# Kernel optimization log

Hardware: AMD Instinct MI355X
Metric: run time of the kernel (lower is better)

## Reference

```python
import jax, jax.numpy as jnp
import numpy as np

IN_FEAT = 3 * 299 * 299  # 268203
D1 = 512
H = 28
OUT = 2


def setup_inputs() -> dict:
    key = jax.random.key(0)
    ks = jax.random.split(key, 10)
    B, T = 4, 64
    s1 = 1.0 / np.sqrt(IN_FEAT)
    s2 = 1.0 / np.sqrt(D1)
    s3 = 1.0 / np.sqrt(H)
    return {
        "x": jax.random.normal(ks[0], (B, T, 3, 299, 299), jnp.float32),
        "W1": jax.random.uniform(ks[1], (IN_FEAT, D1), jnp.float32, -s1, s1),
        "b1": jax.random.uniform(ks[2], (D1,), jnp.float32, -s1, s1),
        "Wi": jax.random.uniform(ks[3], (D1, H), jnp.float32, -s2, s2),
        "Wr": jax.random.uniform(ks[4], (H, H), jnp.float32, -s3, s3),
        "br": jax.random.uniform(ks[5], (H,), jnp.float32, -s3, s3),
        "A": jax.random.normal(ks[6], (H,), jnp.float32),
        "tau": 1.0 + jax.random.uniform(ks[7], (H,), jnp.float32),  # positive time constants
        "W2": jax.random.uniform(ks[8], (H, OUT), jnp.float32, -s3, s3),
        "b2": jax.random.uniform(ks[9], (OUT,), jnp.float32, -s3, s3),
    }


def reference(x, W1, b1, Wi, Wr, br, A, tau, W2, b2):
    B, T = x.shape[0], x.shape[1]
    xf = x.reshape(B, T, -1)                      # [B, T, 268203]
    h1 = jax.nn.relu(jnp.einsum('btf,fd->btd', xf, W1) + b1)  # [B, T, 512]
    u = jnp.einsum('btd,dh->bth', h1, Wi)         # precomputed input drive [B, T, H]
    dt = 1.0

    def step(h, u_t):
        # fused-Euler LTC cell: f gates both time-constant and attractor A
        ft = jax.nn.sigmoid(u_t + h @ Wr + br)
        h_new = (h + dt * ft * A) / (1.0 + dt * (1.0 / tau + ft))
        return h_new, h_new

    h0 = jnp.zeros((B, H), x.dtype)
    _, hs = jax.lax.scan(step, h0, jnp.swapaxes(u, 0, 1))  # [T, B, H]
    last = jax.nn.relu(hs[-1])                    # relu then take last step
    out = last @ W2 + b2                          # [B, 2]
    return jax.nn.sigmoid(out)
```

## Files before the change

### kernel.cpp

```cpp
#include <hip/hip_runtime.h>
#include <hip/hip_bf16.h>

#define KTOT   268203
#define MROWS  256
#define NCOLS  512
#define HDIM   28
#define NSTEPS 8382
#define FSTEP  8381
#define KREM   11
#define BN     256
#define BROWS  40

typedef __attribute__((ext_vector_type(4))) float        f32x4;
typedef __attribute__((ext_vector_type(4))) unsigned int u32x4;
typedef __attribute__((ext_vector_type(8))) __bf16       bf16x8;

static __device__ inline bf16x8 pack8(const float* f) {
    union { bf16x8 v; __hip_bfloat16 h[8]; } u;
    #pragma unroll
    for (int j = 0; j < 8; ++j) u.h[j] = __float2bfloat16(f[j]);
    return u.v;
}
static __device__ inline unsigned short bfbits(float v) {
    __hip_bfloat16 h = __float2bfloat16(v);
    union { __hip_bfloat16 h; unsigned short u; } c; c.h = h; return c.u;
}

__global__ __launch_bounds__(512, 2) void gemm1_kernel(
    const float* __restrict__ x, const float* __restrict__ W1,
    __hip_bfloat16* __restrict__ part, int steps_per, int nks)
{
    __shared__ __align__(16) float          Albuf[3][MROWS * 32];
    __shared__ __align__(16) __hip_bfloat16 Blds[3][BN * BROWS];

    const int tid  = threadIdx.x;
    const int lane = tid & 63;
    const int w    = tid >> 6;
    const int wm   = w >> 1;
    const int wn   = w & 1;

    int bx, ks;
    {
        const int id = blockIdx.x;
        if ((nks & 7) == 0) {
            const int xcd = id & 7;
            const int m_  = id >> 3;
            bx = m_ & 1;
            ks = ((m_ >> 1) << 3) | xcd;
        } else {
            bx = id & 1;
            ks = id >> 1;
        }
    }
    const int bcol = bx * BN;

    const int dlt = lane >> 5;
    const int m   = lane & 31;
    const int rw7 = (2 * w + dlt) & 7;
    const int ag  = (m >> 2) ^ rw7;
    const size_t a_off = (size_t)(2 * w + dlt) * KTOT + ag * 4 + (m & 3);
    const int bkh = w >> 2;
    const int bcl = (w & 3) * 64 + lane;

    f32x4 acc[4][8];
    #pragma unroll
    for (int i = 0; i < 4; ++i)
        #pragma unroll
        for (int j = 0; j < 8; ++j)
            acc[i][j] = (f32x4){0.f, 0.f, 0.f, 0.f};

    const int s0 = ks * steps_per;
    int s1 = s0 + steps_per;
    if (s1 > NSTEPS) s1 = NSTEPS;
    int s1f = (s1 < FSTEP) ? s1 : FSTEP;
    int nfull = s1f - s0;
    if (nfull < 0) nfull = 0;

    float breg[16];

    auto loadB = [&](int s) {
        const float* bp = W1 + ((size_t)s * 32 + bkh * 16) * NCOLS + bcol + bcl;
        #pragma unroll
        for (int kk = 0; kk < 16; ++kk)
            breg[kk] = bp[(size_t)kk * NCOLS];
    };
    auto issueA = [&](int s, int buf) {
        const float* ap = x + a_off + (size_t)s * 32;
        float* lbase = &Albuf[buf][0];
        #pragma unroll
        for (int i = 0; i < 16; ++i) {
            const float* gp = ap + (size_t)i * 16 * KTOT;
            char* lp = (char*)lbase + (i * 8 + w) * 256;
            __builtin_amdgcn_global_load_lds(
                (const __attribute__((address_space(1))) unsigned int*)(const void*)gp,
                (__attribute__((address_space(3))) unsigned int*)(void*)lp, 4, 0, 0);
        }
    };
    auto writeB = [&](int buf) {
        unsigned int pk[8];
        #pragma unroll
        for (int q = 0; q < 8; ++q)
            pk[q] = (unsigned int)bfbits(breg[2 * q]) |
                    ((unsigned int)bfbits(breg[2 * q + 1]) << 16);
        __hip_bfloat16* dst = &Blds[buf][bcl * BROWS + bkh * 16];
        *(u32x4*)(dst)     = (u32x4){pk[0], pk[1], pk[2], pk[3]};
        *(u32x4*)(dst + 8) = (u32x4){pk[4], pk[5], pk[6], pk[7]};
    };

    auto compute = [&](int buf) {
        const int rc = lane & 15, ko = lane >> 4;
        bf16x8 bq[8];
        #pragma unroll
        for (int ni = 0; ni < 8; ++ni)
            bq[ni] = *(const bf16x8*)&Blds[buf][(wn * 128 + ni * 16 + rc) * BROWS + ko * 8];
        const int soff = ((2 * ko) ^ (rc & 7)) * 16;
        const char* abase = (const char*)&Albuf[buf][0];
        #pragma unroll
        for (int mi = 0; mi < 4; ++mi) {
            const int ab = (wm * 64 + mi * 16 + rc) * 128;
            float afv[8];
            *(f32x4*)&afv[0] = *(const f32x4*)(abase + ab + soff);
            *(f32x4*)&afv[4] = *(const f32x4*)(abase + ab + (soff ^ 16));
            const bf16x8 af = pack8(afv);
            #pragma unroll
            for (int ni = 0; ni < 8; ++ni)
                acc[mi][ni] = __builtin_amdgcn_mfma_f32_16x16x32_bf16(
                    af, bq[ni], acc[mi][ni], 0, 0, 0);
        }
    };

    if (nfull > 0) {
        loadB(s0); issueA(s0, 0);
        asm volatile("s_waitcnt vmcnt(16)" ::: "memory");
        __builtin_amdgcn_sched_barrier(0);
        writeB(0);
        if (nfull > 1) { loadB(s0 + 1); issueA(s0 + 1, 1); }
        asm volatile("s_waitcnt lgkmcnt(0)" ::: "memory");
        __builtin_amdgcn_sched_barrier(0);

        int buf = 0;
        for (int t = 0; t < nfull; ++t) {
            if (t + 1 < nfull) { asm volatile("s_waitcnt vmcnt(32)" ::: "memory"); }
            else               { asm volatile("s_waitcnt vmcnt(0)"  ::: "memory"); }
            __builtin_amdgcn_sched_barrier(0);
            __builtin_amdgcn_s_barrier();
            __builtin_amdgcn_sched_barrier(0);
            compute(buf);
            __builtin_amdgcn_sched_barrier(0);
            if (t + 1 < nfull) {
                asm volatile("s_waitcnt vmcnt(16)" ::: "memory");
                __builtin_amdgcn_sched_barrier(0);
                const int nb = (buf == 2) ? 0 : buf + 1;
                writeB(nb);
                if (t + 2 < nfull) {
                    const int nnb = (nb == 2) ? 0 : nb + 1;
                    loadB(s0 + t + 2); issueA(s0 + t + 2, nnb);
                }
                asm volatile("s_waitcnt lgkmcnt(0)" ::: "memory");
                __builtin_amdgcn_sched_barrier(0);
                buf = nb;
            }
        }
    }

    if (s1 > FSTEP && s0 < s1) {
        const int buf = nfull % 3;
        __syncthreads();
        {
            const int row = tid >> 1, half = tid & 1;
            #pragma unroll
            for (int i = 0; i < 16; ++i) {
                const int k = half * 16 + i;
                const float v = (k < KREM)
                    ? x[(size_t)row * KTOT + (size_t)FSTEP * 32 + k] : 0.f;
                Albuf[buf][row * 32 + ((k >> 2) ^ (row & 7)) * 4 + (k & 3)] = v;
            }
        }
        {
            const int c = tid & 255, og = tid >> 8;
            #pragma unroll
            for (int i = 0; i < 16; ++i) {
                const int k = og * 16 + i;
                const float v = (k < KREM)
                    ? W1[(size_t)(FSTEP * 32 + k) * NCOLS + bcol + c] : 0.f;
                Blds[buf][c * BROWS + k] = __float2bfloat16(v);
            }
        }
        __syncthreads();
        compute(buf);
    }

    __hip_bfloat16* outp = part + (size_t)ks * MROWS * NCOLS;
    const int rc = lane & 15, q = lane >> 4;
    #pragma unroll
    for (int mi = 0; mi < 4; ++mi) {
        #pragma unroll
        for (int ni = 0; ni < 8; ++ni) {
            const int col = bcol + wn * 128 + ni * 16 + rc;
            #pragma unroll
            for (int j = 0; j < 4; ++j) {
                const int row = wm * 64 + mi * 16 + q * 4 + j;
                const float v  = acc[mi][ni][j];
                const float vh = __shfl_xor(v, 1);
                if (!(rc & 1)) {
                    const unsigned int pk =
                        (unsigned int)bfbits(v) | ((unsigned int)bfbits(vh) << 16);
                    *(unsigned int*)(outp + (size_t)row * NCOLS + col) = pk;
                }
            }
        }
    }
}

__global__ __launch_bounds__(512) void reduce_u_kernel(
    const __hip_bfloat16* __restrict__ part, const float* __restrict__ b1,
    const float* __restrict__ Wi, float* __restrict__ u, int nks)
{
    __shared__ float h1[NCOLS];
    __shared__ f32x4 red[4][128];
    const int row = blockIdx.x;
    const int tid = threadIdx.x;
    const int c4  = tid & 127;
    const int kk  = tid >> 7;

    const unsigned short* pu = (const unsigned short*)part;
    f32x4 sum = (f32x4){0.f, 0.f, 0.f, 0.f};
    for (int k = kk; k < nks; k += 4) {
        const size_t base = ((size_t)k * MROWS + row) * NCOLS + c4 * 4;
        ushort4 pv = *(const ushort4*)&pu[base];
        union { unsigned int u; float f; } c0, c1, c2, c3;
        c0.u = (unsigned int)pv.x << 16; c1.u = (unsigned int)pv.y << 16;
        c2.u = (unsigned int)pv.z << 16; c3.u = (unsigned int)pv.w << 16;
        sum[0] += c0.f; sum[1] += c1.f; sum[2] += c2.f; sum[3] += c3.f;
    }
    red[kk][c4] = sum;
    __syncthreads();

    if (tid < 128) {
        f32x4 t = red[0][tid] + red[1][tid] + red[2][tid] + red[3][tid];
        const f32x4 bb = *(const f32x4*)&b1[tid * 4];
        t += bb;
        #pragma unroll
        for (int j = 0; j < 4; ++j) h1[tid * 4 + j] = fmaxf(t[j], 0.f);
    }
    __syncthreads();

    const int wv = tid >> 6, lane = tid & 63;
    #pragma unroll
    for (int hh = 0; hh < 4; ++hh) {
        const int h = wv * 4 + hh;
        if (h < HDIM) {
            float p = 0.f;
            #pragma unroll
            for (int dd = 0; dd < 8; ++dd) {
                const int d = lane + dd * 64;
                p += h1[d] * Wi[d * HDIM + h];
            }
            #pragma unroll
            for (int off = 32; off; off >>= 1) p += __shfl_down(p, off);
            if (lane == 0) u[row * HDIM + h] = p;
        }
    }
}

__global__ __launch_bounds__(64) void recur_kernel(
    const float* __restrict__ u, const float* __restrict__ Wr,
    const float* __restrict__ br, const float* __restrict__ Av,
    const float* __restrict__ tau, const float* __restrict__ W2,
    const float* __restrict__ b2, float* __restrict__ out)
{
    const int b = blockIdx.x;
    const int j = threadIdx.x;
    const bool act = j < HDIM;
    const int jj = act ? j : 0;

    float wr[HDIM];
    #pragma unroll
    for (int i = 0; i < HDIM; ++i) wr[i] = act ? Wr[i * HDIM + jj] : 0.f;
    const float brj = act ? br[jj] : 0.f;
    const float Aj  = act ? Av[jj] : 0.f;
    const float itj = act ? (1.f / tau[jj]) : 0.f;

    float uv[64];
    #pragma unroll
    for (int t = 0; t < 64; ++t)
        uv[t] = act ? u[(b * 64 + t) * HDIM + jj] : 0.f;

    float h = 0.f;
    #pragma unroll
    for (int t = 0; t < 64; ++t) {
        float a = uv[t] + brj;
        #pragma unroll
        for (int i = 0; i < HDIM; ++i)
            a += __shfl(h, i) * wr[i];
        const float ft = 1.f / (1.f + expf(-a));
        const float hn = (h + ft * Aj) / (1.f + itj + ft);
        h = act ? hn : 0.f;
    }

    const float r  = act ? fmaxf(h, 0.f) : 0.f;
    float p0 = act ? r * W2[jj * 2 + 0] : 0.f;
    float p1 = act ? r * W2[jj * 2 + 1] : 0.f;
    #pragma unroll
    for (int off = 32; off; off >>= 1) {
        p0 += __shfl_down(p0, off);
        p1 += __shfl_down(p1, off);
    }
    if (j == 0) {
        out[b * 2 + 0] = 1.f / (1.f + expf(-(p0 + b2[0])));
        out[b * 2 + 1] = 1.f / (1.f + expf(-(p1 + b2[1])));
    }
}

extern "C" void kernel_launch(void* const* d_in, const int* in_sizes, int n_in,
                              void* d_out, int out_size, void* d_ws, size_t ws_size,
                              hipStream_t stream)
{
    (void)in_sizes; (void)n_in; (void)out_size;
    const float* x   = (const float*)d_in[0];
    const float* W1  = (const float*)d_in[1];
    const float* b1  = (const float*)d_in[2];
    const float* Wi  = (const float*)d_in[3];
    const float* Wr  = (const float*)d_in[4];
    const float* br  = (const float*)d_in[5];
    const float* Av  = (const float*)d_in[6];
    const float* tau = (const float*)d_in[7];
    const float* W2  = (const float*)d_in[8];
    const float* b2  = (const float*)d_in[9];
    float* out = (float*)d_out;

    const size_t per_split = (size_t)MROWS * NCOLS * sizeof(__hip_bfloat16);
    int nks = 128;
    while (nks > 8 && (size_t)nks * per_split + (1 << 16) > ws_size) nks >>= 1;
    const int steps_per = (NSTEPS + nks - 1) / nks;

    __hip_bfloat16* part = (__hip_bfloat16*)d_ws;
    float* u = (float*)((char*)d_ws + (size_t)nks * per_split);

    gemm1_kernel<<<dim3(2 * nks), 512, 0, stream>>>(x, W1, part, steps_per, nks);
    reduce_u_kernel<<<dim3(MROWS), 512, 0, stream>>>(part, b1, Wi, u, nks);
    recur_kernel<<<dim3(4), 64, 0, stream>>>(u, Wr, br, Av, tau, W2, b2, out);
}
```

Before: 228.9 us.

## Double-buffer B registers and issue next-next loads before compute

The main GEMM loop now keeps two register sets for W1 tiles and alternates between them, with the loop unrolled by two. Loads for step t+2 (both W1 into registers and x into LDS via global_load_lds) are issued before the MFMA compute of step t instead of after it, so memory latency overlaps with compute. This deepens the prefetch pipeline at the cost of 16 more live VGPRs per thread and more outstanding loads, with vmcnt thresholds adjusted to match. The higher register use could lower occupancy.

Result: slower. 252.6 us (+10.4%).

```diff
diff --git a/kernel.cpp b/kernel.cpp
--- a/kernel.cpp
+++ b/kernel.cpp
@@ -76,9 +76,9 @@
     int nfull = s1f - s0;
     if (nfull < 0) nfull = 0;
 
-    float breg[16];
-
-    auto loadB = [&](int s) {
+    float bregA[16], bregB[16];
+
+    auto loadB = [&](int s, float* breg) {
         const float* bp = W1 + ((size_t)s * 32 + bkh * 16) * NCOLS + bcol + bcl;
         #pragma unroll
         for (int kk = 0; kk < 16; ++kk)
@@ -96,7 +96,7 @@
                 (__attribute__((address_space(3))) unsigned int*)(void*)lp, 4, 0, 0);
         }
     };
-    auto writeB = [&](int buf) {
+    auto writeB = [&](const float* breg, int buf) {
         unsigned int pk[8];
         #pragma unroll
         for (int q = 0; q < 8; ++q)
@@ -130,36 +130,61 @@
     };
 
     if (nfull > 0) {
-        loadB(s0); issueA(s0, 0);
+        loadB(s0, bregA); issueA(s0, 0);
         asm volatile("s_waitcnt vmcnt(16)" ::: "memory");
         __builtin_amdgcn_sched_barrier(0);
-        writeB(0);
-        if (nfull > 1) { loadB(s0 + 1); issueA(s0 + 1, 1); }
+        writeB(bregA, 0);
+        if (nfull > 1) { loadB(s0 + 1, bregB); issueA(s0 + 1, 1); }
         asm volatile("s_waitcnt lgkmcnt(0)" ::: "memory");
         __builtin_amdgcn_sched_barrier(0);
 
         int buf = 0;
-        for (int t = 0; t < nfull; ++t) {
+        int t = 0;
+        for (;;) {
             if (t + 1 < nfull) { asm volatile("s_waitcnt vmcnt(32)" ::: "memory"); }
             else               { asm volatile("s_waitcnt vmcnt(0)"  ::: "memory"); }
             __builtin_amdgcn_sched_barrier(0);
             __builtin_amdgcn_s_barrier();
             __builtin_amdgcn_sched_barrier(0);
+            if (t + 2 < nfull) {
+                const int nb2 = (buf >= 1) ? buf - 1 : 2;
+                loadB(s0 + t + 2, bregA); issueA(s0 + t + 2, nb2);
+                __builtin_amdgcn_sched_barrier(0);
+            }
             compute(buf);
             __builtin_amdgcn_sched_barrier(0);
             if (t + 1 < nfull) {
-                asm volatile("s_waitcnt vmcnt(16)" ::: "memory");
-                __builtin_amdgcn_sched_barrier(0);
-                const int nb = (buf == 2) ? 0 : buf + 1;
-                writeB(nb);
-                if (t + 2 < nfull) {
-                    const int nnb = (nb == 2) ? 0 : nb + 1;
-                    loadB(s0 + t + 2); issueA(s0 + t + 2, nnb);
-                }
+                if (t + 2 < nfull) { asm volatile("s_waitcnt vmcnt(48)" ::: "memory"); }
+                else               { asm volatile("s_waitcnt vmcnt(16)" ::: "memory"); }
+                __builtin_amdgcn_sched_barrier(0);
+                writeB(bregB, (buf == 2) ? 0 : buf + 1);
                 asm volatile("s_waitcnt lgkmcnt(0)" ::: "memory");
                 __builtin_amdgcn_sched_barrier(0);
-                buf = nb;
-            }
+            }
+            buf = (buf == 2) ? 0 : buf + 1;
+            if (++t >= nfull) break;
+            if (t + 1 < nfull) { asm volatile("s_waitcnt vmcnt(32)" ::: "memory"); }
+            else               { asm volatile("s_waitcnt vmcnt(0)"  ::: "memory"); }
+            __builtin_amdgcn_sched_barrier(0);
+            __builtin_amdgcn_s_barrier();
+            __builtin_amdgcn_sched_barrier(0);
+            if (t + 2 < nfull) {
+                const int nb2 = (buf >= 1) ? buf - 1 : 2;
+                loadB(s0 + t + 2, bregB); issueA(s0 + t + 2, nb2);
+                __builtin_amdgcn_sched_barrier(0);
+            }
+            compute(buf);
+            __builtin_amdgcn_sched_barrier(0);
+            if (t + 1 < nfull) {
+                if (t + 2 < nfull) { asm volatile("s_waitcnt vmcnt(48)" ::: "memory"); }
+                else               { asm volatile("s_waitcnt vmcnt(16)" ::: "memory"); }
+                __builtin_amdgcn_sched_barrier(0);
+                writeB(bregA, (buf == 2) ? 0 : buf + 1);
+                asm volatile("s_waitcnt lgkmcnt(0)" ::: "memory");
+                __builtin_amdgcn_sched_barrier(0);
+            }
+            buf = (buf == 2) ? 0 : buf + 1;
+            if (++t >= nfull) break;
         }
     }
 
```
